# Optimization experiments

Measured on AMD Instinct MI355X. Metric: run time of the kernel, lower is better.

## Reference

```python
import jax, jax.numpy as jnp
import numpy as np

N = 4096
ADP_DIM = 10
TOPK = 20
EPS = 1e-6


def setup_inputs() -> dict:
    key = jax.random.key(0)
    k1, k2, k3, k4, k5, k6 = jax.random.split(key, 6)
    sparsity_mask = (jax.random.uniform(k1, (N, N)) < 0.01).astype(jnp.float32)
    weights = jax.random.uniform(k2, (N, N), dtype=jnp.float32)
    base_adj = sparsity_mask * weights
    return {
        "x_hist": jax.random.normal(k3, (16, 12, N, 2), dtype=jnp.float32),
        "event": jax.random.normal(k4, (16, 12, N, 1), dtype=jnp.float32),
        "base_adj": base_adj,
        "nodevec1": jax.random.normal(k5, (N, ADP_DIM), dtype=jnp.float32),
        "nodevec2": jax.random.normal(k6, (ADP_DIM, N), dtype=jnp.float32),
        "alpha_logit": jnp.asarray(0.0, dtype=jnp.float32),  # sigmoid(0) = alpha_init 0.5
    }


def reference(x_hist, event, base_adj, nodevec1, nodevec2, alpha_logit):
    n = base_adj.shape[0]
    dt = base_adj.dtype

    # ---- history adjacency: cosine-ish similarity -> relu -> row softmax ----
    feat = x_hist.mean(axis=(0, 1))                                  # [N, C]
    feat = feat / (jnp.linalg.norm(feat, axis=1, keepdims=True) + EPS)
    A_h = jax.nn.softmax(jax.nn.relu(feat @ feat.T), axis=1)         # [N, N]

    # ---- event adjacency (Eq. 7 distance decay) ----
    sev = event.mean(axis=(0, 1))[:, 0]                              # [N]
    impacted = (sev > 0.0).astype(dt)
    dist_mx = (base_adj > 0).astype(dt)
    eta = jnp.exp(-0.5 * dist_mx)
    A_e_raw = sev[:, None] * eta * base_adj                          # [N, N]
    A_e = jax.nn.softmax(jax.nn.relu(A_e_raw), axis=1)
    A_e = jnp.where(impacted.sum() > 0, A_e, jnp.zeros_like(A_e))

    # ---- base + learnable adaptive adjacency ----
    A_adp = jax.nn.softmax(jax.nn.relu(nodevec1 @ nodevec2), axis=1)
    A_base = base_adj + A_adp

    # ---- dynamic fusion (Eq. 9) ----
    gamma = jax.nn.sigmoid(alpha_logit)
    A_dyn = gamma * A_h + (1.0 - gamma) * A_e
    A_dyn = 0.5 * A_dyn + 0.5 * A_base

    # ---- top-k row sparsification ----
    _, idx = jax.lax.top_k(A_dyn, TOPK)                              # [N, k]
    mask = jnp.zeros_like(A_dyn).at[jnp.arange(n)[:, None], idx].set(1.0)
    A_dyn = A_dyn * mask

    # ---- symmetric normalization D^{-1/2}(A+I)D^{-1/2} (broadcast form of diag matmuls) ----
    A = A_dyn + jnp.eye(n, dtype=dt)
    deg = A.sum(axis=1)
    d_inv_sqrt = (deg + EPS) ** -0.5
    d_inv_sqrt = jnp.where(jnp.isinf(d_inv_sqrt), jnp.zeros_like(d_inv_sqrt), d_inv_sqrt)
    return d_inv_sqrt[:, None] * A * d_inv_sqrt[None, :]
```

## Files before the change

kernel.cpp:

```cpp
#include <hip/hip_runtime.h>
#include <math.h>

#define NN 4096
#define KTOP 20
#define EPSF 1e-6f

__device__ __forceinline__ float block_rsumf(float v, volatile float* red) {
#pragma unroll
  for (int o = 1; o < 64; o <<= 1) v += __shfl_xor(v, o, 64);
  __syncthreads();
  if ((threadIdx.x & 63) == 0) red[threadIdx.x >> 6] = v;
  __syncthreads();
  return red[0] + red[1] + red[2] + red[3];
}

__global__ __launch_bounds__(256) void k_prep_a(const float* __restrict__ xh,
    const float* __restrict__ ev, float* __restrict__ psx,
    float* __restrict__ psy, float* __restrict__ pse, int* __restrict__ cnt) {
  if (blockIdx.x == 0 && threadIdx.x == 0) *cnt = 0;
  int ic = blockIdx.x & 15, tc = blockIdx.x >> 4;
  int i = ic * 256 + threadIdx.x;
  const float2* xh2 = (const float2*)xh;
  float sx = 0.f, sy = 0.f, se = 0.f;
  for (int bt = tc * 24; bt < tc * 24 + 24; ++bt) {
    float2 v = xh2[(size_t)bt * NN + i];
    sx += v.x; sy += v.y;
    se += ev[(size_t)bt * NN + i];
  }
  psx[tc * NN + i] = sx; psy[tc * NN + i] = sy; pse[tc * NN + i] = se;
}

__global__ void k_prep_b(const float* __restrict__ psx, const float* __restrict__ psy,
    const float* __restrict__ pse, float2* __restrict__ featn,
    float* __restrict__ sev, int* __restrict__ cnt) {
  int i = blockIdx.x * 256 + threadIdx.x;
  float sx = 0.f, sy = 0.f, se = 0.f;
#pragma unroll
  for (int t = 0; t < 8; ++t) {
    sx += psx[t * NN + i]; sy += psy[t * NN + i]; se += pse[t * NN + i];
  }
  sx *= (1.f / 192.f); sy *= (1.f / 192.f); se *= (1.f / 192.f);
  float nrm = sqrtf(sx * sx + sy * sy) + EPSF;
  featn[i] = make_float2(sx / nrm, sy / nrm);
  sev[i] = se;
  unsigned long long m = __ballot(se > 0.f);
  if ((threadIdx.x & 63) == 0) atomicAdd(cnt, (int)__popcll(m));
}

__global__ __launch_bounds__(256) void k_gemm(const float* __restrict__ nv1,
    const float* __restrict__ nv2, const float* __restrict__ base_adj,
    const float* __restrict__ sev, float* __restrict__ aexp,
    float* __restrict__ aspart, float* __restrict__ edpart) {
  const int lane = threadIdx.x & 63, w = threadIdx.x >> 6;
  const int j = blockIdx.x * 256 + lane * 4;
  const int i0 = blockIdx.y * 64 + w * 16;
  float4 wv[10];
#pragma unroll
  for (int d = 0; d < 10; ++d) wv[d] = *(const float4*)&nv2[d * NN + j];
  for (int it = 0; it < 16; ++it) {
    int i = i0 + it;
    const float* r = nv1 + (size_t)i * 10;
    float4 a = make_float4(0.f, 0.f, 0.f, 0.f);
#pragma unroll
    for (int d = 0; d < 10; ++d) {
      float rd = r[d];
      a.x += rd * wv[d].x; a.y += rd * wv[d].y;
      a.z += rd * wv[d].z; a.w += rd * wv[d].w;
    }
    float4 o;
    o.x = __expf(fmaxf(a.x, 0.f)); o.y = __expf(fmaxf(a.y, 0.f));
    o.z = __expf(fmaxf(a.z, 0.f)); o.w = __expf(fmaxf(a.w, 0.f));
    *(float4*)&aexp[(size_t)i * NN + j] = o;
    float ps = o.x + o.y + o.z + o.w;
    float4 B = *(const float4*)&base_adj[(size_t)i * NN + j];
    float esc = sev[i] * 0.6065306597f;
    float ed = (__expf(fmaxf(esc * B.x, 0.f)) - 1.f) +
               (__expf(fmaxf(esc * B.y, 0.f)) - 1.f) +
               (__expf(fmaxf(esc * B.z, 0.f)) - 1.f) +
               (__expf(fmaxf(esc * B.w, 0.f)) - 1.f);
#pragma unroll
    for (int of = 1; of < 64; of <<= 1) {
      ps += __shfl_xor(ps, of, 64);
      ed += __shfl_xor(ed, of, 64);
    }
    if (lane == 0) {
      aspart[i * 16 + blockIdx.x] = ps;
      edpart[i * 16 + blockIdx.x] = ed;
    }
  }
}

__global__ __launch_bounds__(256) void k_wts(const float2* __restrict__ featn,
    const float* __restrict__ aspart, const float* __restrict__ edpart,
    const float* __restrict__ alpha, const int* __restrict__ cnt,
    float4* __restrict__ wts) {
  const int i0 = blockIdx.x * 4;
  const int tid = threadIdx.x, lane = tid & 63, wv = tid >> 6;
  __shared__ float red[4][4];
  float2 fi0 = featn[i0], fi1 = featn[i0 + 1], fi2 = featn[i0 + 2], fi3 = featn[i0 + 3];
  const float4* f4 = (const float4*)featn;
  float h0 = 0.f, h1 = 0.f, h2 = 0.f, h3 = 0.f;
#pragma unroll
  for (int p = 0; p < 8; ++p) {
    float4 F = f4[p * 256 + tid];
    h0 += __expf(fmaxf(fi0.x * F.x + fi0.y * F.y, 0.f)) +
          __expf(fmaxf(fi0.x * F.z + fi0.y * F.w, 0.f));
    h1 += __expf(fmaxf(fi1.x * F.x + fi1.y * F.y, 0.f)) +
          __expf(fmaxf(fi1.x * F.z + fi1.y * F.w, 0.f));
    h2 += __expf(fmaxf(fi2.x * F.x + fi2.y * F.y, 0.f)) +
          __expf(fmaxf(fi2.x * F.z + fi2.y * F.w, 0.f));
    h3 += __expf(fmaxf(fi3.x * F.x + fi3.y * F.y, 0.f)) +
          __expf(fmaxf(fi3.x * F.z + fi3.y * F.w, 0.f));
  }
#pragma unroll
  for (int o = 1; o < 64; o <<= 1) {
    h0 += __shfl_xor(h0, o, 64); h1 += __shfl_xor(h1, o, 64);
    h2 += __shfl_xor(h2, o, 64); h3 += __shfl_xor(h3, o, 64);
  }
  if (lane == 0) { red[0][wv] = h0; red[1][wv] = h1; red[2][wv] = h2; red[3][wv] = h3; }
  __syncthreads();
  if (tid < 4) {
    int i = i0 + tid;
    float HS = red[tid][0] + red[tid][1] + red[tid][2] + red[tid][3];
    float AS = 0.f, ED = 0.f;
#pragma unroll
    for (int k = 0; k < 16; ++k) {
      AS += aspart[i * 16 + k];
      ED += edpart[i * 16 + k];
    }
    float ES = 4096.f + ED;
    float gamma = 1.f / (1.f + __expf(-alpha[0]));
    float eflag = (*cnt > 0) ? 1.f : 0.f;
    wts[i] = make_float4(0.5f * gamma / HS,
                         0.5f * (1.f - gamma) * eflag / ES,
                         0.5f / AS, 0.f);
  }
}

__device__ __forceinline__ void fb_row(int i, const float (&v)[16], int* kidx,
    float* kval, float* dinv, volatile float* redf, volatile int* redi,
    int* eq_js, int* eq_cnt, int* slot) {
  const int tid = threadIdx.x;
  const int lane = tid & 63, wv = tid >> 6;
  unsigned cur = 0;
  for (int bit = 30; bit >= 0; --bit) {
    float tf = __uint_as_float(cur | (1u << bit));
    int lc = 0;
#pragma unroll
    for (int c = 0; c < 16; ++c) lc += (v[c] >= tf) ? 1 : 0;
#pragma unroll
    for (int o = 1; o < 64; o <<= 1) lc += __shfl_xor(lc, o, 64);
    __syncthreads();
    if (lane == 0) redi[wv] = lc;
    __syncthreads();
    int tot = redi[0] + redi[1] + redi[2] + redi[3];
    if (tot >= KTOP) cur |= (1u << bit);
  }
  float T = __uint_as_float(cur);
  int lgt = 0;
#pragma unroll
  for (int c = 0; c < 16; ++c) lgt += (v[c] > T) ? 1 : 0;
#pragma unroll
  for (int o = 1; o < 64; o <<= 1) lgt += __shfl_xor(lgt, o, 64);
  __syncthreads();
  if (lane == 0) redi[wv] = lgt;
  if (tid == 0) *eq_cnt = 0;
  __syncthreads();
  int cgt = redi[0] + redi[1] + redi[2] + redi[3];

  float lsum = 0.f;
#pragma unroll
  for (int c = 0; c < 16; ++c) {
    if (v[c] > T) {
      int p = atomicAdd(slot, 1);
      kidx[i * KTOP + p] = tid * 16 + c;
      kval[i * KTOP + p] = v[c];
      lsum += v[c];
    } else if (v[c] == T) {
      int p = atomicAdd(eq_cnt, 1);
      if (p < 64) eq_js[p] = tid * 16 + c;
    }
  }
  __syncthreads();
  int need = KTOP - cgt;
  if (tid == 0) {
    int m = *eq_cnt < 64 ? *eq_cnt : 64;
    for (int s = 0; s < need; ++s) {
      int best = s;
      for (int u = s + 1; u < m; ++u)
        if (eq_js[u] < eq_js[best]) best = u;
      int tmp = eq_js[s]; eq_js[s] = eq_js[best]; eq_js[best] = tmp;
      kidx[i * KTOP + cgt + s] = eq_js[s];
      kval[i * KTOP + cgt + s] = T;
    }
  }
  float tot = block_rsumf(lsum, redf);
  if (tid == 0) dinv[i] = 1.f / sqrtf(tot + (float)need * T + 1.f + EPSF);
}

__global__ __launch_bounds__(256) void k_row(
    const float* __restrict__ base_adj, const float* __restrict__ aexp,
    const float2* __restrict__ featn, const float* __restrict__ sev,
    const float4* __restrict__ wts, int* __restrict__ kidx,
    float* __restrict__ kval, float* __restrict__ dinv) {
  const int i = blockIdx.x;
  const int tid = threadIdx.x;
  const int lane = tid & 63, wv = tid >> 6;
  const int j0 = tid * 16;

  __shared__ float maxima[256];
  __shared__ float candV[64];
  __shared__ int candJ[64];
  __shared__ float redf[4];
  __shared__ int redi[4];
  __shared__ int eq_js[64];
  __shared__ int ccnt, wslot, eq_cnt;
  __shared__ float sTT;

  float4 w4 = wts[i];
  const float wh = w4.x, we = w4.y, wa = w4.z;
  float2 fi = featn[i];
  float esc = sev[i] * 0.6065306597f;

  const float4* b4 = (const float4*)(base_adj + (size_t)i * NN + j0);
  const float4* a4 = (const float4*)(aexp + (size_t)i * NN + j0);
  const float4* f4 = (const float4*)featn;

  float v[16];
  float m = 0.f;
#pragma unroll
  for (int q = 0; q < 4; ++q) {
    float4 B = b4[q], A = a4[q];
    float4 F0 = f4[tid * 8 + 2 * q], F1 = f4[tid * 8 + 2 * q + 1];
    float bq[4] = {B.x, B.y, B.z, B.w};
    float aq[4] = {A.x, A.y, A.z, A.w};
    float hq[4];
    hq[0] = __expf(fmaxf(fi.x * F0.x + fi.y * F0.y, 0.f));
    hq[1] = __expf(fmaxf(fi.x * F0.z + fi.y * F0.w, 0.f));
    hq[2] = __expf(fmaxf(fi.x * F1.x + fi.y * F1.y, 0.f));
    hq[3] = __expf(fmaxf(fi.x * F1.z + fi.y * F1.w, 0.f));
#pragma unroll
    for (int s = 0; s < 4; ++s) {
      float val = wh * hq[s] + wa * aq[s] + we + 0.5f * bq[s] +
                  we * (__expf(fmaxf(esc * bq[s], 0.f)) - 1.f);
      v[4 * q + s] = val;
      m = fmaxf(m, val);
    }
  }
  maxima[tid] = m;
  if (tid == 0) { ccnt = 0; wslot = 0; }
  __syncthreads();

  if (wv == 0) {
    float x0 = maxima[lane], x1 = maxima[lane + 64];
    float x2 = maxima[lane + 128], x3 = maxima[lane + 192];
    unsigned cur = 0;
    for (int bit = 30; bit >= 19; --bit) {
      float tf = __uint_as_float(cur | (1u << bit));
      int c_ = __popcll(__ballot(x0 >= tf)) + __popcll(__ballot(x1 >= tf)) +
               __popcll(__ballot(x2 >= tf)) + __popcll(__ballot(x3 >= tf));
      if (c_ >= KTOP) cur |= (1u << bit);
    }
    sTT = __uint_as_float(cur);
  }
  __syncthreads();
  float T0 = sTT;

#pragma unroll
  for (int c = 0; c < 16; ++c) {
    if (v[c] >= T0) {
      int p = atomicAdd(&ccnt, 1);
      if (p < 64) { candV[p] = v[c]; candJ[p] = j0 + c; }
    }
  }
  __syncthreads();
  bool fb = (ccnt > 64);

  if (!fb && wv == 0) {
    int n = ccnt;
    float lv = (lane < n) ? candV[lane] : 0.f;
    int lj = (lane < n) ? candJ[lane] : 0x7FFFFFFF;
    unsigned cur = 0;
    for (int bit = 30; bit >= 0; --bit) {
      float tf = __uint_as_float(cur | (1u << bit));
      if (__popcll(__ballot(lv >= tf)) >= KTOP) cur |= (1u << bit);
    }
    float T = __uint_as_float(cur);
    bool gt = lv > T;
    int cgt = __popcll(__ballot(gt));
    if (gt) {
      int p = atomicAdd(&wslot, 1);
      kidx[i * KTOP + p] = lj;
      kval[i * KTOP + p] = lv;
    }
    int need = KTOP - cgt;
    bool eq = (lv == T);
    for (int k = 0; k < need; ++k) {
      int pj = eq ? lj : 0x7FFFFFFF;
#pragma unroll
      for (int o = 1; o < 64; o <<= 1) {
        int q = __shfl_xor(pj, o, 64);
        pj = q < pj ? q : pj;
      }
      if (lane == 0) {
        kidx[i * KTOP + cgt + k] = pj;
        kval[i * KTOP + cgt + k] = T;
      }
      if (lj == pj) eq = false;
    }
    float ds = gt ? lv : 0.f;
#pragma unroll
    for (int o = 1; o < 64; o <<= 1) ds += __shfl_xor(ds, o, 64);
    if (lane == 0) dinv[i] = 1.f / sqrtf(ds + (float)need * T + 1.f + EPSF);
  }

  if (fb) {
    __syncthreads();
    fb_row(i, v, kidx, kval, dinv, redf, redi, eq_js, &eq_cnt, &wslot);
  }
}

__global__ __launch_bounds__(256) void k_write(
    const int* __restrict__ kidx, const float* __restrict__ kval,
    const float* __restrict__ dinv, float* __restrict__ out) {
  const int i = blockIdx.x;
  const int tid = threadIdx.x;
  __shared__ float row[NN];
  float4* r4 = (float4*)row;
#pragma unroll
  for (int c = 0; c < 4; ++c) r4[c * 256 + tid] = make_float4(0.f, 0.f, 0.f, 0.f);
  __syncthreads();
  if (tid < KTOP) {
    int j = kidx[i * KTOP + tid];
    row[j] = kval[i * KTOP + tid];
  }
  __syncthreads();
  float di = dinv[i];
  const float4* dv4 = (const float4*)dinv;
  float4* o4 = (float4*)out;
#pragma unroll
  for (int c = 0; c < 4; ++c) {
    int j4 = c * 256 + tid;
    float4 rv = r4[j4];
    float4 dv = dv4[j4];
    int jb = j4 * 4;
    float4 o;
    o.x = di * (rv.x + ((jb + 0) == i ? 1.f : 0.f)) * dv.x;
    o.y = di * (rv.y + ((jb + 1) == i ? 1.f : 0.f)) * dv.y;
    o.z = di * (rv.z + ((jb + 2) == i ? 1.f : 0.f)) * dv.z;
    o.w = di * (rv.w + ((jb + 3) == i ? 1.f : 0.f)) * dv.w;
    o4[(size_t)i * (NN / 4) + j4] = o;
  }
}

extern "C" void kernel_launch(void* const* d_in, const int* in_sizes, int n_in,
                              void* d_out, int out_size, void* d_ws, size_t ws_size,
                              hipStream_t stream) {
  const float* xh    = (const float*)d_in[0];
  const float* ev    = (const float*)d_in[1];
  const float* base  = (const float*)d_in[2];
  const float* nv1   = (const float*)d_in[3];
  const float* nv2   = (const float*)d_in[4];
  const float* alpha = (const float*)d_in[5];
  float* out = (float*)d_out;

  char* ws = (char*)d_ws;
  int*    cnt    = (int*)ws;
  float2* featn  = (float2*)(ws + 256);
  float*  sev    = (float*)(ws + 33024);
  float*  dinv   = (float*)(ws + 49408);
  int*    kidx   = (int*)(ws + 65792);
  float*  kval   = (float*)(ws + 393472);
  float4* wts    = (float4*)(ws + 721152);
  float*  psx    = (float*)(ws + 786688);
  float*  psy    = (float*)(ws + 917760);
  float*  pse    = (float*)(ws + 1048832);
  float*  aspart = (float*)(ws + 786688);
  float*  edpart = (float*)(ws + 1048832);

  k_prep_a<<<128, 256, 0, stream>>>(xh, ev, psx, psy, pse, cnt);
  k_prep_b<<<16, 256, 0, stream>>>(psx, psy, pse, featn, sev, cnt);
  k_gemm<<<dim3(16, 64), 256, 0, stream>>>(nv1, nv2, base, sev, out, aspart, edpart);
  k_wts<<<1024, 256, 0, stream>>>(featn, aspart, edpart, alpha, cnt, wts);
  k_row<<<NN, 256, 0, stream>>>(base, out, featn, sev, wts, kidx, kval, dinv);
  k_write<<<NN, 256, 0, stream>>>(kidx, kval, dinv, out);
}
```

Baseline: 90.98 us.

## Retile adaptive-adjacency GEMM, skip base_adj reads for non-impacted rows, LDS-reduce partials

Restructures k_gemm so each block covers 4 rows by 1024 columns on a 4x1024 grid instead of 64 rows by 256 columns. The base_adj tile is now loaded only when the row's event severity is positive, because otherwise the event term is zero. Per-row partial sums go through shared memory before the wave reductions, which leaves 4 partials per row and lets k_wts sum fewer values. This is meant to cut base_adj memory traffic and shrink the partial-sum reduction. In exchange it adds a __syncthreads per block and many more, smaller blocks.

Result: faster. 79.90 us (-12.2%).

```diff
diff --git a/kernel.cpp b/kernel.cpp
--- a/kernel.cpp
+++ b/kernel.cpp
@@ -51,14 +51,21 @@
     const float* __restrict__ nv2, const float* __restrict__ base_adj,
     const float* __restrict__ sev, float* __restrict__ aexp,
     float* __restrict__ aspart, float* __restrict__ edpart) {
-  const int lane = threadIdx.x & 63, w = threadIdx.x >> 6;
-  const int j = blockIdx.x * 256 + lane * 4;
-  const int i0 = blockIdx.y * 64 + w * 16;
+  const int tid = threadIdx.x, lane = tid & 63;
+  const int bx = blockIdx.x;
+  const int i0 = blockIdx.y * 4;
+  const int j = bx * 1024 + tid * 4;
+
+  __shared__ float lps[4][256];
+  __shared__ float led[4][256];
+
   float4 wv[10];
 #pragma unroll
   for (int d = 0; d < 10; ++d) wv[d] = *(const float4*)&nv2[d * NN + j];
-  for (int it = 0; it < 16; ++it) {
-    int i = i0 + it;
+
+#pragma unroll
+  for (int k = 0; k < 4; ++k) {
+    int i = i0 + k;
     const float* r = nv1 + (size_t)i * 10;
     float4 a = make_float4(0.f, 0.f, 0.f, 0.f);
 #pragma unroll
@@ -71,22 +78,34 @@
     o.x = __expf(fmaxf(a.x, 0.f)); o.y = __expf(fmaxf(a.y, 0.f));
     o.z = __expf(fmaxf(a.z, 0.f)); o.w = __expf(fmaxf(a.w, 0.f));
     *(float4*)&aexp[(size_t)i * NN + j] = o;
-    float ps = o.x + o.y + o.z + o.w;
-    float4 B = *(const float4*)&base_adj[(size_t)i * NN + j];
+
+    float ed = 0.f;
     float esc = sev[i] * 0.6065306597f;
-    float ed = (__expf(fmaxf(esc * B.x, 0.f)) - 1.f) +
-               (__expf(fmaxf(esc * B.y, 0.f)) - 1.f) +
-               (__expf(fmaxf(esc * B.z, 0.f)) - 1.f) +
-               (__expf(fmaxf(esc * B.w, 0.f)) - 1.f);
-#pragma unroll
-    for (int of = 1; of < 64; of <<= 1) {
-      ps += __shfl_xor(ps, of, 64);
-      ed += __shfl_xor(ed, of, 64);
-    }
-    if (lane == 0) {
-      aspart[i * 16 + blockIdx.x] = ps;
-      edpart[i * 16 + blockIdx.x] = ed;
-    }
+    if (esc > 0.f) {
+      float4 B = *(const float4*)&base_adj[(size_t)i * NN + j];
+      ed = (__expf(fmaxf(esc * B.x, 0.f)) - 1.f) +
+           (__expf(fmaxf(esc * B.y, 0.f)) - 1.f) +
+           (__expf(fmaxf(esc * B.z, 0.f)) - 1.f) +
+           (__expf(fmaxf(esc * B.w, 0.f)) - 1.f);
+    }
+    lps[k][tid] = o.x + o.y + o.z + o.w;
+    led[k][tid] = ed;
+  }
+  __syncthreads();
+
+  const int w = tid >> 6;
+  float4 x = *(const float4*)&lps[w][lane * 4];
+  float4 y = *(const float4*)&led[w][lane * 4];
+  float pa = (x.x + x.y) + (x.z + x.w);
+  float pe = (y.x + y.y) + (y.z + y.w);
+#pragma unroll
+  for (int o = 1; o < 64; o <<= 1) {
+    pa += __shfl_xor(pa, o, 64);
+    pe += __shfl_xor(pe, o, 64);
+  }
+  if (lane == 0) {
+    aspart[(i0 + w) * 4 + bx] = pa;
+    edpart[(i0 + w) * 4 + bx] = pe;
   }
 }
 
@@ -124,9 +143,9 @@
     float HS = red[tid][0] + red[tid][1] + red[tid][2] + red[tid][3];
     float AS = 0.f, ED = 0.f;
 #pragma unroll
-    for (int k = 0; k < 16; ++k) {
-      AS += aspart[i * 16 + k];
-      ED += edpart[i * 16 + k];
+    for (int k = 0; k < 4; ++k) {
+      AS += aspart[i * 4 + k];
+      ED += edpart[i * 4 + k];
     }
     float ES = 4096.f + ED;
     float gamma = 1.f / (1.f + __expf(-alpha[0]));
@@ -376,11 +395,11 @@
   float*  psy    = (float*)(ws + 917760);
   float*  pse    = (float*)(ws + 1048832);
   float*  aspart = (float*)(ws + 786688);
-  float*  edpart = (float*)(ws + 1048832);
+  float*  edpart = (float*)(ws + 917760);
 
   k_prep_a<<<128, 256, 0, stream>>>(xh, ev, psx, psy, pse, cnt);
   k_prep_b<<<16, 256, 0, stream>>>(psx, psy, pse, featn, sev, cnt);
-  k_gemm<<<dim3(16, 64), 256, 0, stream>>>(nv1, nv2, base, sev, out, aspart, edpart);
+  k_gemm<<<dim3(4, 1024), 256, 0, stream>>>(nv1, nv2, base, sev, out, aspart, edpart);
   k_wts<<<1024, 256, 0, stream>>>(featn, aspart, edpart, alpha, cnt, wts);
   k_row<<<NN, 256, 0, stream>>>(base, out, featn, sev, wts, kidx, kval, dinv);
   k_write<<<NN, 256, 0, stream>>>(kidx, kval, dinv, out);
```

## Fuse adaptive GEMM, row-sum weights and top-k into one per-row-pair kernel

Applied to the files above, without the earlier changes.

Merges k_gemm, k_wts and k_row into a single kernel in which each block handles two rows. It computes the adaptive exp values into LDS instead of writing a 64 MB intermediate to global memory and reading it back. The three row softmax denominators are reduced in-block before the top-k selection, and the event-exp base load is skipped when severity is nonpositive. The cost is 32 KB of LDS per block, which limits occupancy, and recomputing the history exp terms in both passes.

After: 114.9 us. 1.26x slower.

```diff
diff --git a/kernel.cpp b/kernel.cpp
--- a/kernel.cpp
+++ b/kernel.cpp
@@ -47,96 +47,6 @@
   if ((threadIdx.x & 63) == 0) atomicAdd(cnt, (int)__popcll(m));
 }
 
-__global__ __launch_bounds__(256) void k_gemm(const float* __restrict__ nv1,
-    const float* __restrict__ nv2, const float* __restrict__ base_adj,
-    const float* __restrict__ sev, float* __restrict__ aexp,
-    float* __restrict__ aspart, float* __restrict__ edpart) {
-  const int lane = threadIdx.x & 63, w = threadIdx.x >> 6;
-  const int j = blockIdx.x * 256 + lane * 4;
-  const int i0 = blockIdx.y * 64 + w * 16;
-  float4 wv[10];
-#pragma unroll
-  for (int d = 0; d < 10; ++d) wv[d] = *(const float4*)&nv2[d * NN + j];
-  for (int it = 0; it < 16; ++it) {
-    int i = i0 + it;
-    const float* r = nv1 + (size_t)i * 10;
-    float4 a = make_float4(0.f, 0.f, 0.f, 0.f);
-#pragma unroll
-    for (int d = 0; d < 10; ++d) {
-      float rd = r[d];
-      a.x += rd * wv[d].x; a.y += rd * wv[d].y;
-      a.z += rd * wv[d].z; a.w += rd * wv[d].w;
-    }
-    float4 o;
-    o.x = __expf(fmaxf(a.x, 0.f)); o.y = __expf(fmaxf(a.y, 0.f));
-    o.z = __expf(fmaxf(a.z, 0.f)); o.w = __expf(fmaxf(a.w, 0.f));
-    *(float4*)&aexp[(size_t)i * NN + j] = o;
-    float ps = o.x + o.y + o.z + o.w;
-    float4 B = *(const float4*)&base_adj[(size_t)i * NN + j];
-    float esc = sev[i] * 0.6065306597f;
-    float ed = (__expf(fmaxf(esc * B.x, 0.f)) - 1.f) +
-               (__expf(fmaxf(esc * B.y, 0.f)) - 1.f) +
-               (__expf(fmaxf(esc * B.z, 0.f)) - 1.f) +
-               (__expf(fmaxf(esc * B.w, 0.f)) - 1.f);
-#pragma unroll
-    for (int of = 1; of < 64; of <<= 1) {
-      ps += __shfl_xor(ps, of, 64);
-      ed += __shfl_xor(ed, of, 64);
-    }
-    if (lane == 0) {
-      aspart[i * 16 + blockIdx.x] = ps;
-      edpart[i * 16 + blockIdx.x] = ed;
-    }
-  }
-}
-
-__global__ __launch_bounds__(256) void k_wts(const float2* __restrict__ featn,
-    const float* __restrict__ aspart, const float* __restrict__ edpart,
-    const float* __restrict__ alpha, const int* __restrict__ cnt,
-    float4* __restrict__ wts) {
-  const int i0 = blockIdx.x * 4;
-  const int tid = threadIdx.x, lane = tid & 63, wv = tid >> 6;
-  __shared__ float red[4][4];
-  float2 fi0 = featn[i0], fi1 = featn[i0 + 1], fi2 = featn[i0 + 2], fi3 = featn[i0 + 3];
-  const float4* f4 = (const float4*)featn;
-  float h0 = 0.f, h1 = 0.f, h2 = 0.f, h3 = 0.f;
-#pragma unroll
-  for (int p = 0; p < 8; ++p) {
-    float4 F = f4[p * 256 + tid];
-    h0 += __expf(fmaxf(fi0.x * F.x + fi0.y * F.y, 0.f)) +
-          __expf(fmaxf(fi0.x * F.z + fi0.y * F.w, 0.f));
-    h1 += __expf(fmaxf(fi1.x * F.x + fi1.y * F.y, 0.f)) +
-          __expf(fmaxf(fi1.x * F.z + fi1.y * F.w, 0.f));
-    h2 += __expf(fmaxf(fi2.x * F.x + fi2.y * F.y, 0.f)) +
-          __expf(fmaxf(fi2.x * F.z + fi2.y * F.w, 0.f));
-    h3 += __expf(fmaxf(fi3.x * F.x + fi3.y * F.y, 0.f)) +
-          __expf(fmaxf(fi3.x * F.z + fi3.y * F.w, 0.f));
-  }
-#pragma unroll
-  for (int o = 1; o < 64; o <<= 1) {
-    h0 += __shfl_xor(h0, o, 64); h1 += __shfl_xor(h1, o, 64);
-    h2 += __shfl_xor(h2, o, 64); h3 += __shfl_xor(h3, o, 64);
-  }
-  if (lane == 0) { red[0][wv] = h0; red[1][wv] = h1; red[2][wv] = h2; red[3][wv] = h3; }
-  __syncthreads();
-  if (tid < 4) {
-    int i = i0 + tid;
-    float HS = red[tid][0] + red[tid][1] + red[tid][2] + red[tid][3];
-    float AS = 0.f, ED = 0.f;
-#pragma unroll
-    for (int k = 0; k < 16; ++k) {
-      AS += aspart[i * 16 + k];
-      ED += edpart[i * 16 + k];
-    }
-    float ES = 4096.f + ED;
-    float gamma = 1.f / (1.f + __expf(-alpha[0]));
-    float eflag = (*cnt > 0) ? 1.f : 0.f;
-    wts[i] = make_float4(0.5f * gamma / HS,
-                         0.5f * (1.f - gamma) * eflag / ES,
-                         0.5f / AS, 0.f);
-  }
-}
-
 __device__ __forceinline__ void fb_row(int i, const float (&v)[16], int* kidx,
     float* kval, float* dinv, volatile float* redf, volatile int* redi,
     int* eq_js, int* eq_cnt, int* slot) {
@@ -198,125 +108,206 @@
   if (tid == 0) dinv[i] = 1.f / sqrtf(tot + (float)need * T + 1.f + EPSF);
 }
 
-__global__ __launch_bounds__(256) void k_row(
-    const float* __restrict__ base_adj, const float* __restrict__ aexp,
-    const float2* __restrict__ featn, const float* __restrict__ sev,
-    const float4* __restrict__ wts, int* __restrict__ kidx,
+__global__ __launch_bounds__(256) void k_fused(
+    const float* __restrict__ base_adj, const float* __restrict__ nv1,
+    const float* __restrict__ nv2, const float2* __restrict__ featn,
+    const float* __restrict__ sev, const float* __restrict__ alpha,
+    const int* __restrict__ cnt, int* __restrict__ kidx,
     float* __restrict__ kval, float* __restrict__ dinv) {
-  const int i = blockIdx.x;
-  const int tid = threadIdx.x;
-  const int lane = tid & 63, wv = tid >> 6;
+  const int i0 = blockIdx.x * 2;
+  const int tid = threadIdx.x, lane = tid & 63, wv = tid >> 6;
   const int j0 = tid * 16;
 
+  __shared__ float ae[2][NN];
   __shared__ float maxima[256];
   __shared__ float candV[64];
   __shared__ int candJ[64];
-  __shared__ float redf[4];
+  __shared__ float redf[24];
   __shared__ int redi[4];
   __shared__ int eq_js[64];
   __shared__ int ccnt, wslot, eq_cnt;
   __shared__ float sTT;
 
-  float4 w4 = wts[i];
-  const float wh = w4.x, we = w4.y, wa = w4.z;
-  float2 fi = featn[i];
-  float esc = sev[i] * 0.6065306597f;
-
-  const float4* b4 = (const float4*)(base_adj + (size_t)i * NN + j0);
-  const float4* a4 = (const float4*)(aexp + (size_t)i * NN + j0);
+  const float* r0 = nv1 + (size_t)i0 * 10;
+  const float* r1 = r0 + 10;
+  float esc0 = sev[i0] * 0.6065306597f;
+  float esc1 = sev[i0 + 1] * 0.6065306597f;
+  float2 fi0 = featn[i0], fi1 = featn[i0 + 1];
   const float4* f4 = (const float4*)featn;
-
-  float v[16];
-  float m = 0.f;
+  float gamma = 1.f / (1.f + __expf(-alpha[0]));
+  float eflag = (*cnt > 0) ? 1.f : 0.f;
+
+  float as0 = 0.f, as1 = 0.f, ed0 = 0.f, ed1 = 0.f, hs0 = 0.f, hs1 = 0.f;
 #pragma unroll
   for (int q = 0; q < 4; ++q) {
-    float4 B = b4[q], A = a4[q];
-    float4 F0 = f4[tid * 8 + 2 * q], F1 = f4[tid * 8 + 2 * q + 1];
-    float bq[4] = {B.x, B.y, B.z, B.w};
-    float aq[4] = {A.x, A.y, A.z, A.w};
-    float hq[4];
-    hq[0] = __expf(fmaxf(fi.x * F0.x + fi.y * F0.y, 0.f));
-    hq[1] = __expf(fmaxf(fi.x * F0.z + fi.y * F0.w, 0.f));
-    hq[2] = __expf(fmaxf(fi.x * F1.x + fi.y * F1.y, 0.f));
-    hq[3] = __expf(fmaxf(fi.x * F1.z + fi.y * F1.w, 0.f));
-#pragma unroll
-    for (int s = 0; s < 4; ++s) {
-      float val = wh * hq[s] + wa * aq[s] + we + 0.5f * bq[s] +
-                  we * (__expf(fmaxf(esc * bq[s], 0.f)) - 1.f);
-      v[4 * q + s] = val;
-      m = fmaxf(m, val);
-    }
-  }
-  maxima[tid] = m;
-  if (tid == 0) { ccnt = 0; wslot = 0; }
-  __syncthreads();
-
-  if (wv == 0) {
-    float x0 = maxima[lane], x1 = maxima[lane + 64];
-    float x2 = maxima[lane + 128], x3 = maxima[lane + 192];
-    unsigned cur = 0;
-    for (int bit = 30; bit >= 19; --bit) {
-      float tf = __uint_as_float(cur | (1u << bit));
-      int c_ = __popcll(__ballot(x0 >= tf)) + __popcll(__ballot(x1 >= tf)) +
-               __popcll(__ballot(x2 >= tf)) + __popcll(__ballot(x3 >= tf));
-      if (c_ >= KTOP) cur |= (1u << bit);
-    }
-    sTT = __uint_as_float(cur);
-  }
-  __syncthreads();
-  float T0 = sTT;
-
-#pragma unroll
-  for (int c = 0; c < 16; ++c) {
-    if (v[c] >= T0) {
-      int p = atomicAdd(&ccnt, 1);
-      if (p < 64) { candV[p] = v[c]; candJ[p] = j0 + c; }
-    }
-  }
-  __syncthreads();
-  bool fb = (ccnt > 64);
-
-  if (!fb && wv == 0) {
-    int n = ccnt;
-    float lv = (lane < n) ? candV[lane] : 0.f;
-    int lj = (lane < n) ? candJ[lane] : 0x7FFFFFFF;
-    unsigned cur = 0;
-    for (int bit = 30; bit >= 0; --bit) {
-      float tf = __uint_as_float(cur | (1u << bit));
-      if (__popcll(__ballot(lv >= tf)) >= KTOP) cur |= (1u << bit);
-    }
-    float T = __uint_as_float(cur);
-    bool gt = lv > T;
-    int cgt = __popcll(__ballot(gt));
-    if (gt) {
-      int p = atomicAdd(&wslot, 1);
-      kidx[i * KTOP + p] = lj;
-      kval[i * KTOP + p] = lv;
-    }
-    int need = KTOP - cgt;
-    bool eq = (lv == T);
-    for (int k = 0; k < need; ++k) {
-      int pj = eq ? lj : 0x7FFFFFFF;
-#pragma unroll
-      for (int o = 1; o < 64; o <<= 1) {
-        int q = __shfl_xor(pj, o, 64);
-        pj = q < pj ? q : pj;
-      }
-      if (lane == 0) {
-        kidx[i * KTOP + cgt + k] = pj;
-        kval[i * KTOP + cgt + k] = T;
-      }
-      if (lj == pj) eq = false;
-    }
-    float ds = gt ? lv : 0.f;
-#pragma unroll
-    for (int o = 1; o < 64; o <<= 1) ds += __shfl_xor(ds, o, 64);
-    if (lane == 0) dinv[i] = 1.f / sqrtf(ds + (float)need * T + 1.f + EPSF);
-  }
-
-  if (fb) {
-    __syncthreads();
-    fb_row(i, v, kidx, kval, dinv, redf, redi, eq_js, &eq_cnt, &wslot);
+    const int jq = j0 + 4 * q;
+    float4 a0 = make_float4(0.f, 0.f, 0.f, 0.f);
+    float4 a1 = make_float4(0.f, 0.f, 0.f, 0.f);
+#pragma unroll
+    for (int d = 0; d < 10; ++d) {
+      float4 w4 = *(const float4*)&nv2[(size_t)d * NN + jq];
+      float rd0 = r0[d], rd1 = r1[d];
+      a0.x += rd0 * w4.x; a0.y += rd0 * w4.y; a0.z += rd0 * w4.z; a0.w += rd0 * w4.w;
+      a1.x += rd1 * w4.x; a1.y += rd1 * w4.y; a1.z += rd1 * w4.z; a1.w += rd1 * w4.w;
+    }
+    float e;
+    e = __expf(fmaxf(a0.x, 0.f)); ae[0][(4 * q + 0) * 256 + tid] = e; as0 += e;
+    e = __expf(fmaxf(a0.y, 0.f)); ae[0][(4 * q + 1) * 256 + tid] = e; as0 += e;
+    e = __expf(fmaxf(a0.z, 0.f)); ae[0][(4 * q + 2) * 256 + tid] = e; as0 += e;
+    e = __expf(fmaxf(a0.w, 0.f)); ae[0][(4 * q + 3) * 256 + tid] = e; as0 += e;
+    e = __expf(fmaxf(a1.x, 0.f)); ae[1][(4 * q + 0) * 256 + tid] = e; as1 += e;
+    e = __expf(fmaxf(a1.y, 0.f)); ae[1][(4 * q + 1) * 256 + tid] = e; as1 += e;
+    e = __expf(fmaxf(a1.z, 0.f)); ae[1][(4 * q + 2) * 256 + tid] = e; as1 += e;
+    e = __expf(fmaxf(a1.w, 0.f)); ae[1][(4 * q + 3) * 256 + tid] = e; as1 += e;
+
+    if (esc0 > 0.f) {
+      float4 B = *(const float4*)&base_adj[(size_t)i0 * NN + jq];
+      ed0 += (__expf(fmaxf(esc0 * B.x, 0.f)) - 1.f) +
+             (__expf(fmaxf(esc0 * B.y, 0.f)) - 1.f) +
+             (__expf(fmaxf(esc0 * B.z, 0.f)) - 1.f) +
+             (__expf(fmaxf(esc0 * B.w, 0.f)) - 1.f);
+    }
+    if (esc1 > 0.f) {
+      float4 B = *(const float4*)&base_adj[(size_t)(i0 + 1) * NN + jq];
+      ed1 += (__expf(fmaxf(esc1 * B.x, 0.f)) - 1.f) +
+             (__expf(fmaxf(esc1 * B.y, 0.f)) - 1.f) +
+             (__expf(fmaxf(esc1 * B.z, 0.f)) - 1.f) +
+             (__expf(fmaxf(esc1 * B.w, 0.f)) - 1.f);
+    }
+    float4 F0 = f4[(jq >> 1)], F1 = f4[(jq >> 1) + 1];
+    hs0 += __expf(fmaxf(fi0.x * F0.x + fi0.y * F0.y, 0.f)) +
+           __expf(fmaxf(fi0.x * F0.z + fi0.y * F0.w, 0.f)) +
+           __expf(fmaxf(fi0.x * F1.x + fi0.y * F1.y, 0.f)) +
+           __expf(fmaxf(fi0.x * F1.z + fi0.y * F1.w, 0.f));
+    hs1 += __expf(fmaxf(fi1.x * F0.x + fi1.y * F0.y, 0.f)) +
+           __expf(fmaxf(fi1.x * F0.z + fi1.y * F0.w, 0.f)) +
+           __expf(fmaxf(fi1.x * F1.x + fi1.y * F1.y, 0.f)) +
+           __expf(fmaxf(fi1.x * F1.z + fi1.y * F1.w, 0.f));
+  }
+
+#pragma unroll
+  for (int o = 1; o < 64; o <<= 1) {
+    hs0 += __shfl_xor(hs0, o, 64); hs1 += __shfl_xor(hs1, o, 64);
+    as0 += __shfl_xor(as0, o, 64); as1 += __shfl_xor(as1, o, 64);
+    ed0 += __shfl_xor(ed0, o, 64); ed1 += __shfl_xor(ed1, o, 64);
+  }
+  if (lane == 0) {
+    redf[wv * 6 + 0] = hs0; redf[wv * 6 + 1] = hs1;
+    redf[wv * 6 + 2] = as0; redf[wv * 6 + 3] = as1;
+    redf[wv * 6 + 4] = ed0; redf[wv * 6 + 5] = ed1;
+  }
+  __syncthreads();
+  float HS0 = redf[0] + redf[6] + redf[12] + redf[18];
+  float HS1 = redf[1] + redf[7] + redf[13] + redf[19];
+  float AS0 = redf[2] + redf[8] + redf[14] + redf[20];
+  float AS1 = redf[3] + redf[9] + redf[15] + redf[21];
+  float ES0 = 4096.f + redf[4] + redf[10] + redf[16] + redf[22];
+  float ES1 = 4096.f + redf[5] + redf[11] + redf[17] + redf[23];
+
+#pragma unroll 1
+  for (int r = 0; r < 2; ++r) {
+    const int i = i0 + r;
+    const float wh = 0.5f * gamma / (r == 0 ? HS0 : HS1);
+    const float we = 0.5f * (1.f - gamma) * eflag / (r == 0 ? ES0 : ES1);
+    const float wa = 0.5f / (r == 0 ? AS0 : AS1);
+    const float esc = (r == 0) ? esc0 : esc1;
+    const float2 fi = (r == 0) ? fi0 : fi1;
+    const float4* b4 = (const float4*)(base_adj + (size_t)i * NN + j0);
+
+    float v[16];
+    float m = 0.f;
+#pragma unroll
+    for (int q = 0; q < 4; ++q) {
+      float4 B = b4[q];
+      float4 F0 = f4[tid * 8 + 2 * q], F1 = f4[tid * 8 + 2 * q + 1];
+      float bq[4] = {B.x, B.y, B.z, B.w};
+      float hq[4];
+      hq[0] = __expf(fmaxf(fi.x * F0.x + fi.y * F0.y, 0.f));
+      hq[1] = __expf(fmaxf(fi.x * F0.z + fi.y * F0.w, 0.f));
+      hq[2] = __expf(fmaxf(fi.x * F1.x + fi.y * F1.y, 0.f));
+      hq[3] = __expf(fmaxf(fi.x * F1.z + fi.y * F1.w, 0.f));
+#pragma unroll
+      for (int s = 0; s < 4; ++s) {
+        int c = 4 * q + s;
+        float aq = ae[r][c * 256 + tid];
+        float val = wh * hq[s] + wa * aq + we + 0.5f * bq[s] +
+                    we * (__expf(fmaxf(esc * bq[s], 0.f)) - 1.f);
+        v[c] = val;
+        m = fmaxf(m, val);
+      }
+    }
+    maxima[tid] = m;
+    if (tid == 0) { ccnt = 0; wslot = 0; }
+    __syncthreads();
+
+    if (wv == 0) {
+      float x0 = maxima[lane], x1 = maxima[lane + 64];
+      float x2 = maxima[lane + 128], x3 = maxima[lane + 192];
+      unsigned cur = 0;
+      for (int bit = 30; bit >= 19; --bit) {
+        float tf = __uint_as_float(cur | (1u << bit));
+        int c_ = __popcll(__ballot(x0 >= tf)) + __popcll(__ballot(x1 >= tf)) +
+                 __popcll(__ballot(x2 >= tf)) + __popcll(__ballot(x3 >= tf));
+        if (c_ >= KTOP) cur |= (1u << bit);
+      }
+      sTT = __uint_as_float(cur);
+    }
+    __syncthreads();
+    float T0 = sTT;
+
+#pragma unroll
+    for (int c = 0; c < 16; ++c) {
+      if (v[c] >= T0) {
+        int p = atomicAdd(&ccnt, 1);
+        if (p < 64) { candV[p] = v[c]; candJ[p] = j0 + c; }
+      }
+    }
+    __syncthreads();
+    bool fb = (ccnt > 64);
+
+    if (!fb && wv == 0) {
+      int n = ccnt;
+      float lv = (lane < n) ? candV[lane] : 0.f;
+      int lj = (lane < n) ? candJ[lane] : 0x7FFFFFFF;
+      unsigned cur = 0;
+      for (int bit = 30; bit >= 0; --bit) {
+        float tf = __uint_as_float(cur | (1u << bit));
+        if (__popcll(__ballot(lv >= tf)) >= KTOP) cur |= (1u << bit);
+      }
+      float T = __uint_as_float(cur);
+      bool gt = lv > T;
+      int cgt = __popcll(__ballot(gt));
+      if (gt) {
+        int p = atomicAdd(&wslot, 1);
+        kidx[i * KTOP + p] = lj;
+        kval[i * KTOP + p] = lv;
+      }
+      int need = KTOP - cgt;
+      bool eq = (lv == T);
+      for (int k = 0; k < need; ++k) {
+        int pj = eq ? lj : 0x7FFFFFFF;
+#pragma unroll
+        for (int o = 1; o < 64; o <<= 1) {
+          int q2 = __shfl_xor(pj, o, 64);
+          pj = q2 < pj ? q2 : pj;
+        }
+        if (lane == 0) {
+          kidx[i * KTOP + cgt + k] = pj;
+          kval[i * KTOP + cgt + k] = T;
+        }
+        if (lj == pj) eq = false;
+      }
+      float ds = gt ? lv : 0.f;
+#pragma unroll
+      for (int o = 1; o < 64; o <<= 1) ds += __shfl_xor(ds, o, 64);
+      if (lane == 0) dinv[i] = 1.f / sqrtf(ds + (float)need * T + 1.f + EPSF);
+    }
+
+    if (fb) {
+      __syncthreads();
+      fb_row(i, v, kidx, kval, dinv, redf, redi, eq_js, &eq_cnt, &wslot);
+    }
+    __syncthreads();
   }
 }
 
@@ -371,17 +362,13 @@
   float*  dinv   = (float*)(ws + 49408);
   int*    kidx   = (int*)(ws + 65792);
   float*  kval   = (float*)(ws + 393472);
-  float4* wts    = (float4*)(ws + 721152);
-  float*  psx    = (float*)(ws + 786688);
-  float*  psy    = (float*)(ws + 917760);
-  float*  pse    = (float*)(ws + 1048832);
-  float*  aspart = (float*)(ws + 786688);
-  float*  edpart = (float*)(ws + 1048832);
+  float*  psx    = (float*)(ws + 721152);
+  float*  psy    = (float*)(ws + 852224);
+  float*  pse    = (float*)(ws + 983296);
 
   k_prep_a<<<128, 256, 0, stream>>>(xh, ev, psx, psy, pse, cnt);
   k_prep_b<<<16, 256, 0, stream>>>(psx, psy, pse, featn, sev, cnt);
-  k_gemm<<<dim3(16, 64), 256, 0, stream>>>(nv1, nv2, base, sev, out, aspart, edpart);
-  k_wts<<<1024, 256, 0, stream>>>(featn, aspart, edpart, alpha, cnt, wts);
-  k_row<<<NN, 256, 0, stream>>>(base, out, featn, sev, wts, kidx, kval, dinv);
+  k_fused<<<NN / 2, 256, 0, stream>>>(base, nv1, nv2, featn, sev, alpha, cnt,
+                                      kidx, kval, dinv);
   k_write<<<NN, 256, 0, stream>>>(kidx, kval, dinv, out);
 }
```
